# Kernel tuning notes

Hardware: AMD Instinct MI355X
Metric: run time of the kernel (lower is better)

The kernel has to match this reference:

```python
import jax, jax.numpy as jnp
import numpy as np

B, NQ, NK, D, H = 4, 1025, 1024, 1024, 16
C = D // H          # per-head channels = 64
DFF = 1024          # FFN hidden, hard-coded in source
LN_EPS = 1e-5


def setup_inputs() -> dict:
    key = jax.random.key(0)
    ks = jax.random.split(key, 12)
    s = 0.02
    return {
        "q": jax.random.normal(ks[0], (B, NQ, D), jnp.float32),
        "k": jax.random.normal(ks[1], (B, NK, D), jnp.float32),
        "v": jax.random.normal(ks[2], (B, NK, D), jnp.float32),
        "w_qk": jax.random.normal(ks[3], (D, D), jnp.float32) * s,
        "dummy": jax.random.normal(ks[4], (1, D), jnp.float32),
        "w1": jax.random.normal(ks[5], (C, C // 2), jnp.float32) * s,
        "b1": jnp.zeros((C // 2,), jnp.float32),
        "w2": jax.random.normal(ks[6], (C, C // 2), jnp.float32) * s,
        "b2": jnp.zeros((C // 2,), jnp.float32),
        "w3": jax.random.normal(ks[7], (2 * C, C), jnp.float32) * s,
        "b3": jnp.zeros((C,), jnp.float32),
        "fw1": jax.random.normal(ks[8], (C, DFF), jnp.float32) * s,
        "fb1": jnp.zeros((DFF,), jnp.float32),
        "fw2": jax.random.normal(ks[9], (DFF, C), jnp.float32) * s,
        "fb2": jnp.zeros((C,), jnp.float32),
        "ln_g": jnp.ones((C,), jnp.float32),
        "ln_b": jnp.zeros((C,), jnp.float32),
    }


def _split_heads(x):
    # 'b n (h c) -> (b h) n c'
    b, n, _ = x.shape
    return x.reshape(b, n, H, C).transpose(0, 2, 1, 3).reshape(b * H, n, C)


def _l2norm(x):
    n = jnp.linalg.norm(x, axis=-1, keepdims=True)
    return x / jnp.maximum(n, 1e-12)


def reference(q, k, v, w_qk, dummy, w1, b1, w2, b2, w3, b3,
              fw1, fb1, fw2, fb2, ln_g, ln_b):
    b, nq, d = q.shape
    residual = q
    qp = q @ w_qk
    kp = jnp.concatenate(
        [k @ w_qk, jnp.broadcast_to(dummy[None], (b, 1, d))], axis=1)
    vp = jnp.concatenate([v, jnp.zeros((b, 1, d), v.dtype)], axis=1)

    qh, kh, vh, rh = map(_split_heads, (qp, kp, vp, residual))

    # cosine-similarity attention, ReLU instead of softmax (dropout p=0)
    attn = jnp.einsum('bic,bjc->bij', _l2norm(qh), _l2norm(kh))
    attn = jax.nn.relu(attn)
    out = jnp.einsum('bij,bjc->bic', attn, vh)  # (b*h, nq, c)

    o1 = jax.nn.relu((out * rh) @ w1 + b1)
    o2 = jax.nn.relu((rh - out) @ w2 + b2)
    o = jnp.concatenate([o1, o2, rh], axis=-1) @ w3 + b3

    # FFN with residual + LayerNorm (dropouts are identity at p=0)
    t = o + rh
    t = t + (jax.nn.relu(t @ fw1 + fb1) @ fw2 + fb2)
    mu = jnp.mean(t, axis=-1, keepdims=True)
    var = jnp.mean(jnp.square(t - mu), axis=-1, keepdims=True)
    t = (t - mu) / jnp.sqrt(var + LN_EPS) * ln_g + ln_b

    t = t + vh  # requires nq == nk + 1

    # '(b h) n c -> b n (h c)'
    return t.reshape(b, H, nq, C).transpose(0, 2, 1, 3).reshape(b, nq, d)
```

## Files before the change

### kernel.cpp

```cpp
#include <hip/hip_runtime.h>
#include <hip/hip_bf16.h>

#define DEV __device__ __forceinline__

typedef __attribute__((ext_vector_type(4))) float  f32x4;
typedef __attribute__((ext_vector_type(8))) short  s16x8;
typedef __attribute__((ext_vector_type(8))) __bf16 bf16x8;

#define NQ   1025
#define BH   64
#define NPAD 1152
#define MT   65600
#define DFF  1024

DEV short f2bf(float f){
  unsigned u = __builtin_bit_cast(unsigned, f);
  u = u + 0x7fffu + ((u >> 16) & 1u);
  return (short)(u >> 16);
}
DEV float bf2f(short s){
  unsigned u = ((unsigned)(unsigned short)s) << 16;
  return __builtin_bit_cast(float, u);
}
DEV f32x4 zero4(){ f32x4 z; z[0]=0.f; z[1]=0.f; z[2]=0.f; z[3]=0.f; return z; }
DEV s16x8 zero8(){ s16x8 z; for(int e=0;e<8;e++) z[e]=0; return z; }

DEV f32x4 mfma16(s16x8 a, s16x8 b, f32x4 c){
  return __builtin_amdgcn_mfma_f32_16x16x32_bf16(
      __builtin_bit_cast(bf16x8, a), __builtin_bit_cast(bf16x8, b), c, 0, 0, 0);
}

DEV void gll16(const void* g, void* l){
  __builtin_amdgcn_global_load_lds((const __attribute__((address_space(1))) void*)g,
                                   (__attribute__((address_space(3))) void*)l, 16, 0, 0);
}

DEV s16x8 lds_frag(const char* base, int row, int k8){
  int byte = row*128 + k8*2; byte ^= (row & 7) << 4;
  return *(const s16x8*)(base + byte);
}
DEV void lds_write16(char* base, int row, int k8, s16x8 v){
  int byte = row*128 + k8*2; byte ^= (row & 7) << 4;
  *(s16x8*)(base + byte) = v;
}
DEV void lds_write2(char* base, int row, int col, short v){
  int byte = row*128 + col*2; byte ^= (row & 7) << 4;
  *(short*)(base + byte) = v;
}
DEV void lds_w16_256(char* base, int row, int col, s16x8 v){
  int byte = row*256 + col*2; byte ^= (row & 7) << 4;
  *(s16x8*)(base + byte) = v;
}
DEV s16x8 lds_r16_256(const char* base, int row, int col){
  int byte = row*256 + col*2; byte ^= (row & 7) << 4;
  return *(const s16x8*)(base + byte);
}
DEV void lds_w2_256(char* base, int row, int col, short v){
  int byte = row*256 + col*2; byte ^= (row & 7) << 4;
  *(short*)(base + byte) = v;
}
DEV void blob_w16(char* blob, int row, int k8, s16x8 v){
  int byte = row*128 + k8*2; byte ^= (row & 7) << 4;
  *(s16x8*)(blob + byte) = v;
}

__global__ void k_tcvt(const float* __restrict__ in, int irs, int rin,
                       short* __restrict__ out, int ors){
  __shared__ float tile[32][33];
  int r0 = blockIdx.x*32, c0 = blockIdx.y*32;
  int tx = threadIdx.x, ty = threadIdx.y;
  for (int i=ty;i<32;i+=8){
    int r = r0+i;
    tile[i][tx] = (r < rin) ? in[(long)r*irs + c0 + tx] : 0.f;
  }
  __syncthreads();
  for (int i=ty;i<32;i+=8)
    out[(long)(c0+i)*ors + r0 + tx] = f2bf(tile[tx][i]);
}

__global__ __launch_bounds__(256)
void k_cvtA(const float* __restrict__ q, const float* __restrict__ kk, char* __restrict__ ab){
  int mt = blockIdx.x, kt = blockIdx.y;
  int tid = threadIdx.x;
  int r = tid>>1, ks = (tid&1)*32;
  int pr = mt*128 + r;
  int part = pr >= 4608;
  int pp = part ? pr-4608 : pr;
  int b = pp/NPAD, i = pp%NPAD;
  const float* src = nullptr;
  if (!part && i < 1025) src = q  + ((long)(b*1025+i))*1024 + kt*64 + ks;
  if ( part && i < 1024) src = kk + ((long)(b*1024+i))*1024 + kt*64 + ks;
  char* blob = ab + ((long)(mt*16+kt))*16384;
  #pragma unroll
  for (int c8=0;c8<32;c8+=8){
    s16x8 vv = zero8();
    if (src){
      f32x4 f0 = *(const f32x4*)(src + c8);
      f32x4 f1 = *(const f32x4*)(src + c8 + 4);
      #pragma unroll
      for(int e=0;e<4;e++){ vv[e]=f2bf(f0[e]); vv[4+e]=f2bf(f1[e]); }
    }
    blob_w16(blob, r, ks+c8, vv);
  }
}

__global__ __launch_bounds__(256)
void k_cvtW(const float* __restrict__ w, char* __restrict__ wb){
  __shared__ float T[64][129];
  int nt = blockIdx.x, kt = blockIdx.y;
  int tid = threadIdx.x;
  for (int idx=tid; idx<8192; idx+=256){
    int kr = idx>>7, nc = idx&127;
    T[kr][nc] = w[(long)(kt*64+kr)*1024 + nt*128+nc];
  }
  __syncthreads();
  int r = tid>>1, ks=(tid&1)*32;
  char* blob = wb + ((long)(nt*16+kt))*16384;
  #pragma unroll
  for (int c8=0;c8<32;c8+=8){
    s16x8 vv;
    #pragma unroll
    for(int e=0;e<8;e++) vv[e] = f2bf(T[ks+c8+e][r]);
    blob_w16(blob, r, ks+c8, vv);
  }
}

__global__ __launch_bounds__(256)
void k_cvtV(const float* __restrict__ v, char* __restrict__ vb){
  __shared__ float T[64][65];
  int jt = blockIdx.x, bh = blockIdx.y;
  int b = bh>>4, h = bh&15;
  int tid=threadIdx.x;
  for (int idx=tid; idx<4096; idx+=256){
    int jr = idx>>6, cc = idx&63;
    int j = jt*64+jr;
    T[jr][cc] = (j<1024)? v[((long)(b*1024+j))*1024 + h*64+cc] : 0.f;
  }
  __syncthreads();
  int r = tid>>2, js=(tid&3)*16;
  char* blob = vb + ((long)(bh*18+jt))*8192;
  #pragma unroll
  for (int c8=0;c8<16;c8+=8){
    s16x8 vv;
    #pragma unroll
    for(int e=0;e<8;e++) vv[e] = f2bf(T[js+c8+e][r]);
    blob_w16(blob, r, js+c8, vv);
  }
}

__global__ __launch_bounds__(256,2)
void k_proj(const char* __restrict__ ab, const char* __restrict__ wb,
            char* __restrict__ qpB, char* __restrict__ kpB,
            float* __restrict__ qnorm, float* __restrict__ knorm){
  __shared__ char SM[32768];
  char* A = SM; char* Bm = SM+16384;
  int flat = blockIdx.x;
  int g = (flat&7)*72 + (flat>>3);
  int mt = g>>3, nt = g&7;
  int tid=threadIdx.x, lane=tid&63, wv=tid>>6, lr=lane&15, lg=lane>>4;
  f32x4 acc[4][4];
  for(int a=0;a<4;a++) for(int b=0;b<4;b++) acc[a][b]=zero4();
  int wm=(wv>>1)*64, wn=(wv&1)*64;
  for (int kt=0; kt<16; kt++){
    const char* asrc = ab + ((long)(mt*16+kt))*16384 + wv*4096 + lane*16;
    const char* bsrc = wb + ((long)(nt*16+kt))*16384 + wv*4096 + lane*16;
    char* adst = A + wv*4096;  char* bdst = Bm + wv*4096;
    #pragma unroll
    for (int t=0;t<4;t++){
      gll16(asrc + t*1024, adst + t*1024);
      gll16(bsrc + t*1024, bdst + t*1024);
    }
    __syncthreads();
    #pragma unroll
    for (int kc=0;kc<64;kc+=32){
      int lk = kc + (lg<<3);
      s16x8 af[4], bfr[4];
      #pragma unroll
      for(int i=0;i<4;i++) af[i]  = lds_frag(A,  wm + i*16 + lr, lk);
      #pragma unroll
      for(int i=0;i<4;i++) bfr[i] = lds_frag(Bm, wn + i*16 + lr, lk);
      #pragma unroll
      for(int mi=0;mi<4;mi++)
        #pragma unroll
        for(int ni=0;ni<4;ni++) acc[mi][ni] = mfma16(af[mi], bfr[ni], acc[mi][ni]);
    }
    __syncthreads();
  }
  int head = nt*2 + (wv&1);
  #pragma unroll
  for(int mi=0;mi<4;mi++)
  #pragma unroll
  for(int j=0;j<4;j++){
    float ss = 0.f;
    #pragma unroll
    for(int ni=0;ni<4;ni++){ float x=acc[mi][ni][j]; ss += x*x; }
    ss += __shfl_xor(ss,1); ss += __shfl_xor(ss,2);
    ss += __shfl_xor(ss,4); ss += __shfl_xor(ss,8);
    if (lr==0){
      int pr = mt*128 + wm + mi*16 + lg*4 + j;
      int part = pr>=4608; int pp = part? pr-4608:pr;
      int b = pp/NPAD, i = pp%NPAD;
      float scv = 1.f/fmaxf(sqrtf(ss), 1e-12f);
      (part? knorm : qnorm)[(b*16+head)*NPAD + i] = scv;
    }
  }
  #pragma unroll
  for(int mi=0;mi<4;mi++)
  #pragma unroll
  for(int ni=0;ni<4;ni++)
  #pragma unroll
  for(int j=0;j<4;j++)
    lds_w2_256(SM, wm+mi*16+lg*4+j, wn+ni*16+lr, f2bf(acc[mi][ni][j]));
  __syncthreads();
  {
    int r = tid>>1, half = tid&1;
    int pr = mt*128 + r;
    int part = pr>=4608; int pp = part? pr-4608:pr;
    int b = pp/NPAD, i = pp%NPAD;
    int h2 = nt*2 + half;
    char* dst = (part? kpB : qpB) + ((long)((b*16+h2)*18 + (i>>6)))*8192;
    int rr = i&63;
    #pragma unroll
    for (int c8=0;c8<64;c8+=8){
      s16x8 vv = lds_r16_256(SM, r, half*64 + c8);
      blob_w16(dst, rr, c8, vv);
    }
  }
}

__global__ __launch_bounds__(256,2)
void k_attn(const char* __restrict__ qpB, const char* __restrict__ kpB,
            const char* __restrict__ vtB,
            const float* __restrict__ qnorm, const float* __restrict__ knorm,
            short* __restrict__ att){
  __shared__ char SM[49152];
  char* Q = SM; char* KT = SM+16384; char* VT = KT+8192; char* P = VT+8192;
  int flat = blockIdx.x;
  int g = (flat&7)*72 + (flat>>3);
  int bh = g/9, it = g%9;
  int i0 = it*128;
  int tid=threadIdx.x, lane=tid&63, wv=tid>>6, lr=lane&15, lg=lane>>4;
  {
    const char* src = qpB + ((long)(bh*18 + it*2))*8192 + wv*4096 + lane*16;
    char* dst = Q + wv*4096;
    #pragma unroll
    for (int t=0;t<4;t++) gll16(src + t*1024, dst + t*1024);
  }
  float rq[2][4];
  #pragma unroll
  for(int mi=0;mi<2;mi++)
  #pragma unroll
  for(int j=0;j<4;j++)
    rq[mi][j] = qnorm[bh*NPAD + i0 + wv*32+mi*16+lg*4+j];
  f32x4 oacc[2][4];
  for(int a=0;a<2;a++) for(int b=0;b<4;b++) oacc[a][b]=zero4();
  for (int jt=0; jt<18; ++jt){
    {
      const char* ks = kpB + ((long)(bh*18+jt))*8192 + wv*2048 + lane*16;
      const char* vs = vtB + ((long)(bh*18+jt))*8192 + wv*2048 + lane*16;
      gll16(ks,      KT + wv*2048);
      gll16(ks+1024, KT + wv*2048 + 1024);
      gll16(vs,      VT + wv*2048);
      gll16(vs+1024, VT + wv*2048 + 1024);
    }
    float rk[4];
    #pragma unroll
    for(int ni=0;ni<4;ni++) rk[ni] = knorm[bh*NPAD + jt*64 + ni*16+lr];
    __syncthreads();
    f32x4 sc[2][4];
    for(int a=0;a<2;a++) for(int b=0;b<4;b++) sc[a][b]=zero4();
    #pragma unroll
    for(int kc=0;kc<64;kc+=32){
      int lk = kc + (lg<<3);
      s16x8 af[2], bfr[4];
      #pragma unroll
      for(int i=0;i<2;i++) af[i]=lds_frag(Q, wv*32 + i*16 + lr, lk);
      #pragma unroll
      for(int i=0;i<4;i++) bfr[i]=lds_frag(KT, i*16 + lr, lk);
      #pragma unroll
      for(int mi=0;mi<2;mi++)
        #pragma unroll
        for(int ni=0;ni<4;ni++) sc[mi][ni]=mfma16(af[mi],bfr[ni],sc[mi][ni]);
    }
    #pragma unroll
    for(int mi=0;mi<2;mi++)
    #pragma unroll
    for(int ni=0;ni<4;ni++)
    #pragma unroll
    for(int j=0;j<4;j++){
      float x = sc[mi][ni][j] * rq[mi][j] * rk[ni];
      x = x>0.f?x:0.f;
      lds_write2(P, wv*32 + mi*16 + lg*4 + j, ni*16 + lr, f2bf(x));
    }
    __syncthreads();
    #pragma unroll
    for(int kc=0;kc<64;kc+=32){
      int lk = kc + (lg<<3);
      s16x8 pf[2], vf[4];
      #pragma unroll
      for(int i=0;i<2;i++) pf[i]=lds_frag(P, wv*32 + i*16 + lr, lk);
      #pragma unroll
      for(int i=0;i<4;i++) vf[i]=lds_frag(VT, i*16 + lr, lk);
      #pragma unroll
      for(int mi=0;mi<2;mi++)
        #pragma unroll
        for(int ni=0;ni<4;ni++) oacc[mi][ni]=mfma16(pf[mi],vf[ni],oacc[mi][ni]);
    }
    __syncthreads();
  }
  char* OS = SM+16384;
  #pragma unroll
  for(int mi=0;mi<2;mi++)
  #pragma unroll
  for(int ni=0;ni<4;ni++)
  #pragma unroll
  for(int j=0;j<4;j++)
    lds_write2(OS, wv*32+mi*16+lg*4+j, ni*16+lr, f2bf(oacc[mi][ni][j]));
  __syncthreads();
  {
    int r = tid>>1, half = tid&1;
    int i = i0 + r;
    if (i < 1025){
      short* dst = att + ((long)bh*1025 + i)*64 + half*32;
      #pragma unroll
      for (int u=0; u<32; u+=8){
        s16x8 vv = lds_frag(OS, r, half*32 + u);
        *(s16x8*)(dst + u) = vv;
      }
    }
  }
}

__global__ __launch_bounds__(256,2)
void k_tail(const short* __restrict__ att, const float* __restrict__ q,
    const float* __restrict__ w1, const float* __restrict__ b1,
    const float* __restrict__ w2, const float* __restrict__ b2,
    const float* __restrict__ w3, const float* __restrict__ b3,
    const short* __restrict__ f1T, const short* __restrict__ f2T,
    const float* __restrict__ fb1, const float* __restrict__ fb2,
    const float* __restrict__ ln_g, const float* __restrict__ ln_b,
    const float* __restrict__ v, float* __restrict__ out){
  __shared__ char SM[81920];
  char* R1 = SM;
  char* R2 = SM + 16384;
  char* R3 = SM + 32768;
  char* WP = SM + 49152;
  long m0 = (long)blockIdx.x*128;
  int tid=threadIdx.x, lane=tid&63, wv=tid>>6, lr=lane&15, lg=lane>>4;
  for (int idx=tid; idx<2048; idx+=256){
    int n=idx>>6, c=idx&63;
    lds_write2(WP,      n, c, f2bf(w1[c*32+n]));
    lds_write2(WP+4096, n, c, f2bf(w2[c*32+n]));
  }
  for (int idx=tid; idx<8192; idx+=256){
    int n=idx>>7, kx=idx&127;
    lds_w2_256(WP+8192, n, kx, f2bf(w3[kx*64+n]));
  }
  {
    int r = tid>>1, ks=(tid&1)*32;
    long m = m0 + r;
    if (m < MT){
      int bh=(int)(m/1025); int i=(int)(m-(long)bh*1025); int b=bh>>4, h=bh&15;
      const short* asrc = att + m*64 + ks;
      const float* qsrc = q + ((long)b*1025+i)*1024 + h*64 + ks;
      #pragma unroll
      for (int c8=0;c8<32;c8+=8){
        s16x8 av = *(const s16x8*)(asrc + c8);
        f32x4 q0 = *(const f32x4*)(qsrc + c8);
        f32x4 q1 = *(const f32x4*)(qsrc + c8 + 4);
        s16x8 x1v,x2v,rhv;
        #pragma unroll
        for(int e=0;e<4;e++){
          float o0=bf2f(av[e]),   r0=q0[e];
          float o1=bf2f(av[4+e]), r1=q1[e];
          x1v[e]=f2bf(o0*r0);   x1v[4+e]=f2bf(o1*r1);
          x2v[e]=f2bf(r0-o0);   x2v[4+e]=f2bf(r1-o1);
          rhv[e]=f2bf(r0);      rhv[4+e]=f2bf(r1);
        }
        lds_write16(R1, r, ks+c8, x1v);
        lds_write16(R2, r, ks+c8, x2v);
        lds_write16(R3, r, ks+c8, rhv);
      }
    } else {
      s16x8 z = zero8();
      #pragma unroll
      for (int c8=0;c8<32;c8+=8){
        lds_write16(R1, r, ks+c8, z);
        lds_write16(R2, r, ks+c8, z);
        lds_write16(R3, r, ks+c8, z);
      }
    }
  }
  __syncthreads();
  f32x4 a1[2][4];
  for(int a=0;a<2;a++) for(int b=0;b<4;b++) a1[a][b]=zero4();
  #pragma unroll
  for (int kc=0;kc<64;kc+=32){
    int lk = kc + (lg<<3);
    s16x8 af1[2], af2[2], bw1[2], bw2[2];
    #pragma unroll
    for(int i=0;i<2;i++){
      af1[i]=lds_frag(R1, wv*32+i*16+lr, lk);
      af2[i]=lds_frag(R2, wv*32+i*16+lr, lk);
      bw1[i]=lds_frag(WP,      i*16+lr, lk);
      bw2[i]=lds_frag(WP+4096, i*16+lr, lk);
    }
    #pragma unroll
    for(int mi=0;mi<2;mi++){
      #pragma unroll
      for(int ni=0;ni<2;ni++){
        a1[mi][ni]   = mfma16(af1[mi], bw1[ni], a1[mi][ni]);
        a1[mi][2+ni] = mfma16(af2[mi], bw2[ni], a1[mi][2+ni]);
      }
    }
  }
  float bias12[4];
  #pragma unroll
  for(int ni=0;ni<4;ni++){ int cc=ni*16+lr; bias12[ni] = (cc<32)? b1[cc] : b2[cc-32]; }
  #pragma unroll
  for(int mi=0;mi<2;mi++)
  #pragma unroll
  for(int ni=0;ni<4;ni++)
  #pragma unroll
  for(int j=0;j<4;j++){
    float x = a1[mi][ni][j] + bias12[ni];
    x = x>0.f?x:0.f;
    lds_write2(R1, wv*32+mi*16+lg*4+j, ni*16+lr, f2bf(x));
  }
  f32x4 a2[2][4];
  for(int a=0;a<2;a++) for(int b=0;b<4;b++) a2[a][b]=zero4();
  #pragma unroll
  for (int kc=0;kc<64;kc+=32){
    int lk = kc + (lg<<3);
    s16x8 ao[2], ar[2], bo[4], br[4];
    #pragma unroll
    for(int i=0;i<2;i++){
      ao[i]=lds_frag(R1, wv*32+i*16+lr, lk);
      ar[i]=lds_frag(R3, wv*32+i*16+lr, lk);
    }
    #pragma unroll
    for(int i=0;i<4;i++){
      bo[i]=lds_r16_256(WP+8192, i*16+lr, lk);
      br[i]=lds_r16_256(WP+8192, i*16+lr, 64+lk);
    }
    #pragma unroll
    for(int mi=0;mi<2;mi++)
      #pragma unroll
      for(int ni=0;ni<4;ni++){
        a2[mi][ni]=mfma16(ao[mi],bo[ni],a2[mi][ni]);
        a2[mi][ni]=mfma16(ar[mi],br[ni],a2[mi][ni]);
      }
  }
  float tv[2][4][4];
  {
    float b3v[4];
    #pragma unroll
    for(int ni=0;ni<4;ni++) b3v[ni] = b3[ni*16+lr];
    #pragma unroll
    for(int mi=0;mi<2;mi++)
    #pragma unroll
    for(int j=0;j<4;j++){
      long m = m0 + wv*32+mi*16+lg*4+j;
      int bh=0,i=0,b=0,h=0; const float* qsrc = nullptr;
      if (m < MT){ bh=(int)(m/1025); i=(int)(m-(long)bh*1025); b=bh>>4; h=bh&15;
                   qsrc = q + ((long)b*1025+i)*1024 + h*64; }
      #pragma unroll
      for(int ni=0;ni<4;ni++){
        int cc = ni*16+lr;
        float rh = qsrc ? qsrc[cc] : 0.f;
        float t = a2[mi][ni][j] + b3v[ni] + rh;
        tv[mi][ni][j] = t;
        lds_write2(R2, wv*32+mi*16+lg*4+j, cc, f2bf(t));
      }
    }
  }
  __syncthreads();
  {
    const char* f1 = (const char*)f1T;
    const char* f2 = (const char*)f2T;
    #pragma unroll
    for (int t=0;t<2;t++){
      int seg = wv + t*4;
      int o = seg*1024 + lane*16;
      int r = o>>7, wb = o&127;
      int swb = wb ^ ((r&7)<<4);
      gll16(f1 + r*128 + swb,        WP + o);
      gll16(f2 + (long)r*2048 + swb, WP + 16384 + o);
    }
  }
  __syncthreads();
  f32x4 acc2[2][4];
  for(int a=0;a<2;a++) for(int b=0;b<4;b++) acc2[a][b]=zero4();
  int p = 0;
  for (int d=0; d<16; ++d){
    if (d < 15){
      const char* f1 = (const char*)f1T;
      const char* f2 = (const char*)f2T;
      int dn = d+1, pn = p^1;
      #pragma unroll
      for (int t=0;t<2;t++){
        int seg = wv + t*4;
        int o = seg*1024 + lane*16;
        int r = o>>7, wb = o&127;
        int swb = wb ^ ((r&7)<<4);
        gll16(f1 + (long)dn*8192 + r*128 + swb, WP + pn*8192 + o);
        gll16(f2 + (long)r*2048 + dn*128 + swb, WP + 16384 + pn*8192 + o);
      }
    }
    f32x4 sc[2][4];
    for(int a=0;a<2;a++) for(int b=0;b<4;b++) sc[a][b]=zero4();
    #pragma unroll
    for(int kc=0;kc<64;kc+=32){
      int lk = kc + (lg<<3);
      s16x8 af[2], bfr[4];
      #pragma unroll
      for(int i=0;i<2;i++) af[i]=lds_frag(R2, wv*32+i*16+lr, lk);
      #pragma unroll
      for(int i=0;i<4;i++) bfr[i]=lds_frag(WP + p*8192, i*16+lr, lk);
      #pragma unroll
      for(int mi=0;mi<2;mi++)
        #pragma unroll
        for(int ni=0;ni<4;ni++) sc[mi][ni]=mfma16(af[mi],bfr[ni],sc[mi][ni]);
    }
    #pragma unroll
    for(int mi=0;mi<2;mi++)
    #pragma unroll
    for(int ni=0;ni<4;ni++)
    #pragma unroll
    for(int j=0;j<4;j++){
      int uc = ni*16+lr;
      float x = sc[mi][ni][j] + fb1[d*64+uc];
      x = x>0.f?x:0.f;
      lds_write2(R3, wv*32+mi*16+lg*4+j, uc, f2bf(x));
    }
    #pragma unroll
    for(int kc=0;kc<64;kc+=32){
      int lk = kc + (lg<<3);
      s16x8 uf[2], wf[4];
      #pragma unroll
      for(int i=0;i<2;i++) uf[i]=lds_frag(R3, wv*32+i*16+lr, lk);
      #pragma unroll
      for(int i=0;i<4;i++) wf[i]=lds_frag(WP + 16384 + p*8192, i*16+lr, lk);
      #pragma unroll
      for(int mi=0;mi<2;mi++)
        #pragma unroll
        for(int ni=0;ni<4;ni++) acc2[mi][ni]=mfma16(uf[mi],wf[ni],acc2[mi][ni]);
    }
    __syncthreads();
    p ^= 1;
  }
  #pragma unroll
  for(int mi=0;mi<2;mi++){
    float xv[4][4];
    long mbase = m0 + wv*32 + mi*16 + lg*4;
    #pragma unroll
    for(int ni=0;ni<4;ni++)
    #pragma unroll
    for(int j=0;j<4;j++){
      int c = ni*16+lr;
      xv[ni][j] = acc2[mi][ni][j] + fb2[c] + tv[mi][ni][j];
    }
    #pragma unroll
    for(int j=0;j<4;j++){
      float s = xv[0][j]+xv[1][j]+xv[2][j]+xv[3][j];
      #pragma unroll
      for(int mm=1;mm<16;mm<<=1) s += __shfl_xor(s, mm);
      float mu = s*(1.f/64.f);
      float vs = 0.f;
      #pragma unroll
      for(int ni=0;ni<4;ni++){ float d2=xv[ni][j]-mu; vs += d2*d2; }
      #pragma unroll
      for(int mm=1;mm<16;mm<<=1) vs += __shfl_xor(vs, mm);
      float inv = rsqrtf(vs*(1.f/64.f) + 1e-5f);
      long m = mbase + j;
      if (m < MT){
        int bh = (int)(m/1025); int i = (int)(m - (long)bh*1025);
        int b = bh>>4, h = bh&15;
        #pragma unroll
        for(int ni=0;ni<4;ni++){
          int c = ni*16+lr;
          float y = (xv[ni][j]-mu)*inv*ln_g[c] + ln_b[c];
          float vh = (i<1024)? v[((long)b*1024 + i)*1024 + h*64 + c] : 0.f;
          out[((long)b*1025 + i)*1024 + h*64 + c] = y + vh;
        }
      }
    }
  }
}

extern "C" void kernel_launch(void* const* d_in, const int* in_sizes, int n_in,
                              void* d_out, int out_size, void* d_ws, size_t ws_size,
                              hipStream_t stream) {
  const float* q    = (const float*)d_in[0];
  const float* k    = (const float*)d_in[1];
  const float* v    = (const float*)d_in[2];
  const float* w_qk = (const float*)d_in[3];
  const float* w1   = (const float*)d_in[5];
  const float* b1   = (const float*)d_in[6];
  const float* w2   = (const float*)d_in[7];
  const float* b2   = (const float*)d_in[8];
  const float* w3   = (const float*)d_in[9];
  const float* b3   = (const float*)d_in[10];
  const float* fw1  = (const float*)d_in[11];
  const float* fb1  = (const float*)d_in[12];
  const float* fw2  = (const float*)d_in[13];
  const float* fb2  = (const float*)d_in[14];
  const float* ln_g = (const float*)d_in[15];
  const float* ln_b = (const float*)d_in[16];
  float* out = (float*)d_out;

  char* ws = (char*)d_ws;
  const size_t OFF_A   = 0;
  const size_t SZ_A    = 25190400;
  const size_t OFF_WB  = OFF_A + SZ_A;
  const size_t OFF_F1T = OFF_WB  + (size_t)8*16*16384;
  const size_t OFF_F2T = OFF_F1T + (size_t)1024*64*2;
  const size_t OFF_VT  = OFF_F2T + (size_t)64*1024*2;
  const size_t OFF_QP  = OFF_VT  + (size_t)64*18*8192;
  const size_t OFF_KP  = OFF_QP  + (size_t)64*18*8192;
  const size_t OFF_QN  = OFF_KP  + (size_t)64*18*8192;
  const size_t OFF_KN  = OFF_QN  + (size_t)BH*NPAD*4;
  const size_t NEEDED  = OFF_KN  + (size_t)BH*NPAD*4;
  if (ws_size < NEEDED) return;

  char*  ab   = ws + OFF_A;
  short* att  = (short*)(ws + OFF_A);
  char*  wb   = ws + OFF_WB;
  short* f1T  = (short*)(ws + OFF_F1T);
  short* f2T  = (short*)(ws + OFF_F2T);
  char*  vtB  = ws + OFF_VT;
  char*  qpB  = ws + OFF_QP;
  char*  kpB  = ws + OFF_KP;
  float* qnorm= (float*)(ws + OFF_QN);
  float* knorm= (float*)(ws + OFF_KN);

  k_cvtA<<<dim3(72,16), 256, 0, stream>>>(q, k, ab);
  k_cvtW<<<dim3(8,16),  256, 0, stream>>>(w_qk, wb);
  k_cvtV<<<dim3(18,64), 256, 0, stream>>>(v, vtB);
  k_tcvt<<<dim3(2,32),  dim3(32,8), 0, stream>>>(fw1, 1024, 64,  f1T, 64);
  k_tcvt<<<dim3(32,2),  dim3(32,8), 0, stream>>>(fw2, 64,  1024, f2T, 1024);
  k_proj<<<576, 256, 0, stream>>>(ab, wb, qpB, kpB, qnorm, knorm);
  k_attn<<<576, 256, 0, stream>>>(qpB, kpB, vtB, qnorm, knorm, att);
  k_tail<<<513, 256, 0, stream>>>(att, q, w1, b1, w2, b2, w3, b3,
                                  f1T, f2T, fb1, fb2, ln_g, ln_b, v, out);
}
```

Baseline: 214.6 us.

## Read tail-kernel weights directly from global memory instead of staging in LDS

```diff
diff --git a/kernel.cpp b/kernel.cpp
--- a/kernel.cpp
+++ b/kernel.cpp
@@ -76,6 +76,19 @@
   __syncthreads();
   for (int i=ty;i<32;i+=8)
     out[(long)(c0+i)*ors + r0 + tx] = f2bf(tile[tx][i]);
+}
+
+__global__ __launch_bounds__(256)
+void k_cvtWt(const float* __restrict__ w1, const float* __restrict__ w2,
+             const float* __restrict__ w3, short* __restrict__ wtl){
+  int tid = blockIdx.x*256 + threadIdx.x;
+  if (tid < 2048){
+    int n=tid>>6, c=tid&63; wtl[n*64+c] = f2bf(w1[c*32+n]);
+  } else if (tid < 4096){
+    int t=tid-2048; int n=t>>6, c=t&63; wtl[2048 + n*64+c] = f2bf(w2[c*32+n]);
+  } else if (tid < 12288){
+    int t=tid-4096; int n=t>>7, kx=t&127; wtl[4096 + n*128+kx] = f2bf(w3[kx*64+n]);
+  }
 }
 
 __global__ __launch_bounds__(256)
@@ -331,31 +344,23 @@
   }
 }
 
-__global__ __launch_bounds__(256,2)
+__global__ __launch_bounds__(256,3)
 void k_tail(const short* __restrict__ att, const float* __restrict__ q,
-    const float* __restrict__ w1, const float* __restrict__ b1,
-    const float* __restrict__ w2, const float* __restrict__ b2,
-    const float* __restrict__ w3, const float* __restrict__ b3,
+    const float* __restrict__ b1, const float* __restrict__ b2,
+    const float* __restrict__ b3, const short* __restrict__ wtl,
     const short* __restrict__ f1T, const short* __restrict__ f2T,
     const float* __restrict__ fb1, const float* __restrict__ fb2,
     const float* __restrict__ ln_g, const float* __restrict__ ln_b,
     const float* __restrict__ v, float* __restrict__ out){
-  __shared__ char SM[81920];
+  __shared__ char SM[49152];
   char* R1 = SM;
   char* R2 = SM + 16384;
   char* R3 = SM + 32768;
-  char* WP = SM + 49152;
+  const short* w1T = wtl;
+  const short* w2T = wtl + 2048;
+  const short* w3T = wtl + 4096;
   long m0 = (long)blockIdx.x*128;
   int tid=threadIdx.x, lane=tid&63, wv=tid>>6, lr=lane&15, lg=lane>>4;
-  for (int idx=tid; idx<2048; idx+=256){
-    int n=idx>>6, c=idx&63;
-    lds_write2(WP,      n, c, f2bf(w1[c*32+n]));
-    lds_write2(WP+4096, n, c, f2bf(w2[c*32+n]));
-  }
-  for (int idx=tid; idx<8192; idx+=256){
-    int n=idx>>7, kx=idx&127;
-    lds_w2_256(WP+8192, n, kx, f2bf(w3[kx*64+n]));
-  }
   {
     int r = tid>>1, ks=(tid&1)*32;
     long m = m0 + r;
@@ -391,7 +396,6 @@
       }
     }
   }
-  __syncthreads();
   f32x4 a1[2][4];
   for(int a=0;a<2;a++) for(int b=0;b<4;b++) a1[a][b]=zero4();
   #pragma unroll
@@ -402,8 +406,8 @@
     for(int i=0;i<2;i++){
       af1[i]=lds_frag(R1, wv*32+i*16+lr, lk);
       af2[i]=lds_frag(R2, wv*32+i*16+lr, lk);
-      bw1[i]=lds_frag(WP,      i*16+lr, lk);
-      bw2[i]=lds_frag(WP+4096, i*16+lr, lk);
+      bw1[i]=*(const s16x8*)(w1T + (i*16+lr)*64 + lk);
+      bw2[i]=*(const s16x8*)(w2T + (i*16+lr)*64 + lk);
     }
     #pragma unroll
     for(int mi=0;mi<2;mi++){
@@ -440,8 +444,8 @@
     }
     #pragma unroll
     for(int i=0;i<4;i++){
-      bo[i]=lds_r16_256(WP+8192, i*16+lr, lk);
-      br[i]=lds_r16_256(WP+8192, i*16+lr, 64+lk);
+      bo[i]=*(const s16x8*)(w3T + (i*16+lr)*128 + lk);
+      br[i]=*(const s16x8*)(w3T + (i*16+lr)*128 + 64 + lk);
     }
     #pragma unroll
     for(int mi=0;mi<2;mi++)
@@ -461,9 +465,11 @@
     #pragma unroll
     for(int j=0;j<4;j++){
       long m = m0 + wv*32+mi*16+lg*4+j;
-      int bh=0,i=0,b=0,h=0; const float* qsrc = nullptr;
-      if (m < MT){ bh=(int)(m/1025); i=(int)(m-(long)bh*1025); b=bh>>4; h=bh&15;
-                   qsrc = q + ((long)b*1025+i)*1024 + h*64; }
+      const float* qsrc = nullptr;
+      if (m < MT){
+        int bh=(int)(m/1025); int i=(int)(m-(long)bh*1025); int b=bh>>4, h=bh&15;
+        qsrc = q + ((long)b*1025+i)*1024 + h*64;
+      }
       #pragma unroll
       for(int ni=0;ni<4;ni++){
         int cc = ni*16+lr;
@@ -474,39 +480,12 @@
       }
     }
   }
-  __syncthreads();
-  {
-    const char* f1 = (const char*)f1T;
-    const char* f2 = (const char*)f2T;
-    #pragma unroll
-    for (int t=0;t<2;t++){
-      int seg = wv + t*4;
-      int o = seg*1024 + lane*16;
-      int r = o>>7, wb = o&127;
-      int swb = wb ^ ((r&7)<<4);
-      gll16(f1 + r*128 + swb,        WP + o);
-      gll16(f2 + (long)r*2048 + swb, WP + 16384 + o);
-    }
-  }
-  __syncthreads();
   f32x4 acc2[2][4];
   for(int a=0;a<2;a++) for(int b=0;b<4;b++) acc2[a][b]=zero4();
-  int p = 0;
   for (int d=0; d<16; ++d){
-    if (d < 15){
-      const char* f1 = (const char*)f1T;
-      const char* f2 = (const char*)f2T;
-      int dn = d+1, pn = p^1;
-      #pragma unroll
-      for (int t=0;t<2;t++){
-        int seg = wv + t*4;
-        int o = seg*1024 + lane*16;
-        int r = o>>7, wb = o&127;
-        int swb = wb ^ ((r&7)<<4);
-        gll16(f1 + (long)dn*8192 + r*128 + swb, WP + pn*8192 + o);
-        gll16(f2 + (long)r*2048 + dn*128 + swb, WP + 16384 + pn*8192 + o);
-      }
-    }
+    float fbv[4];
+    #pragma unroll
+    for(int ni=0;ni<4;ni++) fbv[ni] = fb1[d*64 + ni*16+lr];
     f32x4 sc[2][4];
     for(int a=0;a<2;a++) for(int b=0;b<4;b++) sc[a][b]=zero4();
     #pragma unroll
@@ -516,7 +495,7 @@
       #pragma unroll
       for(int i=0;i<2;i++) af[i]=lds_frag(R2, wv*32+i*16+lr, lk);
       #pragma unroll
-      for(int i=0;i<4;i++) bfr[i]=lds_frag(WP + p*8192, i*16+lr, lk);
+      for(int i=0;i<4;i++) bfr[i]=*(const s16x8*)(f1T + (long)(d*64 + i*16+lr)*64 + lk);
       #pragma unroll
       for(int mi=0;mi<2;mi++)
         #pragma unroll
@@ -528,10 +507,9 @@
     for(int ni=0;ni<4;ni++)
     #pragma unroll
     for(int j=0;j<4;j++){
-      int uc = ni*16+lr;
-      float x = sc[mi][ni][j] + fb1[d*64+uc];
+      float x = sc[mi][ni][j] + fbv[ni];
       x = x>0.f?x:0.f;
-      lds_write2(R3, wv*32+mi*16+lg*4+j, uc, f2bf(x));
+      lds_write2(R3, wv*32+mi*16+lg*4+j, ni*16+lr, f2bf(x));
     }
     #pragma unroll
     for(int kc=0;kc<64;kc+=32){
@@ -540,14 +518,12 @@
       #pragma unroll
       for(int i=0;i<2;i++) uf[i]=lds_frag(R3, wv*32+i*16+lr, lk);
       #pragma unroll
-      for(int i=0;i<4;i++) wf[i]=lds_frag(WP + 16384 + p*8192, i*16+lr, lk);
+      for(int i=0;i<4;i++) wf[i]=*(const s16x8*)(f2T + (long)(i*16+lr)*1024 + d*64 + lk);
       #pragma unroll
       for(int mi=0;mi<2;mi++)
         #pragma unroll
         for(int ni=0;ni<4;ni++) acc2[mi][ni]=mfma16(uf[mi],wf[ni],acc2[mi][ni]);
     }
-    __syncthreads();
-    p ^= 1;
   }
   #pragma unroll
   for(int mi=0;mi<2;mi++){
@@ -620,7 +596,8 @@
   const size_t OFF_KP  = OFF_QP  + (size_t)64*18*8192;
   const size_t OFF_QN  = OFF_KP  + (size_t)64*18*8192;
   const size_t OFF_KN  = OFF_QN  + (size_t)BH*NPAD*4;
-  const size_t NEEDED  = OFF_KN  + (size_t)BH*NPAD*4;
+  const size_t OFF_WTL = OFF_KN  + (size_t)BH*NPAD*4;
+  const size_t NEEDED  = OFF_WTL + (size_t)12288*2;
   if (ws_size < NEEDED) return;
 
   char*  ab   = ws + OFF_A;
@@ -633,14 +610,16 @@
   char*  kpB  = ws + OFF_KP;
   float* qnorm= (float*)(ws + OFF_QN);
   float* knorm= (float*)(ws + OFF_KN);
+  short* wtl  = (short*)(ws + OFF_WTL);
 
   k_cvtA<<<dim3(72,16), 256, 0, stream>>>(q, k, ab);
   k_cvtW<<<dim3(8,16),  256, 0, stream>>>(w_qk, wb);
   k_cvtV<<<dim3(18,64), 256, 0, stream>>>(v, vtB);
   k_tcvt<<<dim3(2,32),  dim3(32,8), 0, stream>>>(fw1, 1024, 64,  f1T, 64);
   k_tcvt<<<dim3(32,2),  dim3(32,8), 0, stream>>>(fw2, 64,  1024, f2T, 1024);
+  k_cvtWt<<<48, 256, 0, stream>>>(w1, w2, w3, wtl);
   k_proj<<<576, 256, 0, stream>>>(ab, wb, qpB, kpB, qnorm, knorm);
   k_attn<<<576, 256, 0, stream>>>(qpB, kpB, vtB, qnorm, knorm, att);
-  k_tail<<<513, 256, 0, stream>>>(att, q, w1, b1, w2, b2, w3, b3,
+  k_tail<<<513, 256, 0, stream>>>(att, q, b1, b2, b3, wtl,
                                   f1T, f2T, fb1, fb2, ln_g, ln_b, v, out);
 }
```

Measured after the change: 241.4 us. 1.12x slower.
